# Performance work log

Hardware: AMD Instinct MI355X
Metric: run time of the kernel (lower is better)

Reference implementation:

```python
import jax, jax.numpy as jnp
import numpy as np

NUM_USERS = 50000
NUM_ITEMS = 100000
EMB_DIM = 64
N_LAYERS = 3
N_EDGES = 1200000
N_NODES = NUM_USERS + NUM_ITEMS


def setup_inputs() -> dict:
    key = jax.random.key(0)
    k1, k2, k3, k4, k5 = jax.random.split(key, 5)
    user_emb = jax.random.normal(k1, (NUM_USERS, EMB_DIM), dtype=jnp.float32)
    item_emb = jax.random.normal(k2, (NUM_ITEMS, EMB_DIM), dtype=jnp.float32)
    adj_rows = jax.random.randint(k3, (N_EDGES,), 0, N_NODES, dtype=jnp.int32)
    adj_cols = jax.random.randint(k4, (N_EDGES,), 0, N_NODES, dtype=jnp.int32)
    adj_vals = jax.random.uniform(k5, (N_EDGES,), dtype=jnp.float32)
    return {"user_emb": user_emb, "item_emb": item_emb,
            "adj_rows": adj_rows, "adj_cols": adj_cols, "adj_vals": adj_vals}


def reference(user_emb, item_emb, adj_rows, adj_cols, adj_vals):
    num_users = user_emb.shape[0]
    n_nodes = num_users + item_emb.shape[0]

    def spmm(x):
        # y[r] += v * x[c] for each nnz (r, c, v)  -- COO SpMM
        msgs = adj_vals[:, None] * x[adj_cols]          # [E, D]
        return jax.ops.segment_sum(msgs, adj_rows, num_segments=n_nodes)

    all_emb = jnp.concatenate([user_emb, item_emb], axis=0)  # [N, D]
    # fused multi-hop propagation: accumulate layer outputs instead of stacking
    acc = all_emb
    for _ in range(N_LAYERS):
        all_emb = spmm(all_emb)
        acc = acc + all_emb
    final_embs = acc / jnp.float32(N_LAYERS + 1)  # mean over (n_layers+1) hops
    users = final_embs[:num_users]
    items = final_embs[num_users:]
    return (users, items)
```

## Files before the change

kernel.cpp:

```cpp
#include <hip/hip_runtime.h>
#include <hip/hip_cooperative_groups.h>

namespace cg = cooperative_groups;

#define EMB 64
#define BKT_BITS 9
#define BKT_ROWS (1 << BKT_BITS)
#define BKT_CAP 4608
#define MAX_BKT 512
#define CO_EDGES 2048

typedef float f32x4 __attribute__((ext_vector_type(4)));
typedef int int4e __attribute__((ext_vector_type(4), aligned(8)));


__device__ __forceinline__ const float4* xrow(const float* xu,
                                              const float* xi,
                                              int nu, int col) {
    return (const float4*)((col < nu) ? (xu + (size_t)col * EMB)
                                      : (xi + (size_t)(col - nu) * EMB));
}

__device__ void coarse_body(const int* __restrict__ rows,
                            const int* __restrict__ cols,
                            const float* __restrict__ vals,
                            int* bcur, int2* __restrict__ es_raw,
                            int n_edges, int nbkt,
                            int* lcnt, int* lbase,
                            int cstart, int cstride) {
    int tid = threadIdx.x;
    int nchunk = (n_edges + CO_EDGES - 1) / CO_EDGES;
    for (int c = cstart; c < nchunk; c += cstride) {
        for (int i = tid; i < nbkt; i += 512) lcnt[i] = 0;
        __syncthreads();
        int e0 = c * CO_EDGES;
        int e1 = min(e0 + CO_EDGES, n_edges);
        for (int e = e0 + tid; e < e1; e += 512)
            atomicAdd(&lcnt[rows[e] >> BKT_BITS], 1);
        __syncthreads();
        for (int i = tid; i < nbkt; i += 512) {
            int cc = lcnt[i];
            lbase[i] = cc ? atomicAdd(&bcur[i], cc) : 0;
        }
        __syncthreads();
        for (int e = e0 + tid; e < e1; e += 512) {
            int r = rows[e];
            int b = r >> BKT_BITS;
            int p = atomicAdd(&lbase[b], 1);
            if (p < BKT_CAP)
                es_raw[(size_t)b * BKT_CAP + p] =
                    make_int2(cols[e] | ((r & (BKT_ROWS - 1)) << 18),
                              __float_as_int(vals[e]));
        }
        __syncthreads();
    }
}

__device__ void fine_body(const int* bcur,
                          const int2* __restrict__ es_raw,
                          int2* __restrict__ es,
                          int2* __restrict__ rbe, int n_nodes, int nbkt,
                          int* rcnt, int* rsc,
                          int bstart, int bstride) {
    int tid = threadIdx.x;
    for (int b = bstart; b < nbkt; b += bstride) {
        int cnt = min(bcur[b], BKT_CAP);
        int base = b * BKT_CAP;
        rcnt[tid] = 0;
        __syncthreads();
        for (int j = tid; j < cnt; j += BKT_ROWS)
            atomicAdd(&rcnt[es_raw[base + j].x >> 18], 1);
        __syncthreads();
        int v = rcnt[tid];
        rsc[tid] = v;
        __syncthreads();
        for (int d = 1; d < BKT_ROWS; d <<= 1) {
            int t = (tid >= d) ? rsc[tid - d] : 0;
            __syncthreads();
            rsc[tid] += t;
            __syncthreads();
        }
        int excl = rsc[tid] - v;
        rcnt[tid] = excl;
        int r = (b << BKT_BITS) + tid;
        if (r < n_nodes) rbe[r] = make_int2(base + excl, base + excl + v);
        __syncthreads();
        for (int j = tid; j < cnt; j += BKT_ROWS) {
            int2 e = es_raw[base + j];
            int p = atomicAdd(&rcnt[e.x >> 18], 1);
            es[base + p] = make_int2(e.x & 0x3FFFF, e.y);
        }
        __syncthreads();
    }
}

__device__ void spmm_body(const int2* __restrict__ rbe,
                          const int2* __restrict__ es,
                          const float* xu, const float* xi, int nu,
                          float4* y, const float4* y1, const float4* y2,
                          const float* __restrict__ x0u,
                          const float* __restrict__ x0i,
                          int n_nodes, int mode, int gid0, int gstride) {
    int lanes = n_nodes * 16;
    for (int gid = gid0; gid < lanes; gid += gstride) {
        int r = gid >> 4;
        int q = gid & 15;
        int2 be = rbe[r];
        int beg = be.x;
        int end = be.y;
        float4 a = make_float4(0.f, 0.f, 0.f, 0.f);
        int j = beg;
        for (; j + 4 <= end; j += 4) {
            int4e p01 = *(const int4e*)(es + j);
            int4e p23 = *(const int4e*)(es + j + 2);
            const float4* r0 = xrow(xu, xi, nu, p01.x);
            const float4* r1 = xrow(xu, xi, nu, p01.z);
            const float4* r2 = xrow(xu, xi, nu, p23.x);
            const float4* r3 = xrow(xu, xi, nu, p23.z);
            float4 x0 = r0[q];
            float4 x1 = r1[q];
            float4 x2 = r2[q];
            float4 x3 = r3[q];
            float v0 = __int_as_float(p01.y);
            float v1 = __int_as_float(p01.w);
            float v2 = __int_as_float(p23.y);
            float v3 = __int_as_float(p23.w);
            a.x += v0 * x0.x; a.y += v0 * x0.y; a.z += v0 * x0.z; a.w += v0 * x0.w;
            a.x += v1 * x1.x; a.y += v1 * x1.y; a.z += v1 * x1.z; a.w += v1 * x1.w;
            a.x += v2 * x2.x; a.y += v2 * x2.y; a.z += v2 * x2.z; a.w += v2 * x2.w;
            a.x += v3 * x3.x; a.y += v3 * x3.y; a.z += v3 * x3.z; a.w += v3 * x3.w;
        }
        if (j + 2 <= end) {
            int4e p01 = *(const int4e*)(es + j);
            const float4* r0 = xrow(xu, xi, nu, p01.x);
            const float4* r1 = xrow(xu, xi, nu, p01.z);
            float4 x0 = r0[q];
            float4 x1 = r1[q];
            float v0 = __int_as_float(p01.y);
            float v1 = __int_as_float(p01.w);
            a.x += v0 * x0.x; a.y += v0 * x0.y; a.z += v0 * x0.z; a.w += v0 * x0.w;
            a.x += v1 * x1.x; a.y += v1 * x1.y; a.z += v1 * x1.z; a.w += v1 * x1.w;
            j += 2;
        }
        if (j < end) {
            int2 e0 = es[j];
            float4 x0 = xrow(xu, xi, nu, e0.x)[q];
            float v0 = __int_as_float(e0.y);
            a.x += v0 * x0.x; a.y += v0 * x0.y; a.z += v0 * x0.z; a.w += v0 * x0.w;
        }
        size_t o = (size_t)r * (EMB / 4) + q;
        if (mode < 2) {
            y[o] = a;
        } else {
            const float4* b0 = (r < nu)
                ? ((const float4*)x0u + (size_t)r * (EMB / 4))
                : ((const float4*)x0i + (size_t)(r - nu) * (EMB / 4));
            float4 f0 = b0[q];
            float4 a1 = y1[o];
            float4 a2 = y2[o];
            float4 ac;
            ac.x = 0.25f * (f0.x + a1.x + a2.x + a.x);
            ac.y = 0.25f * (f0.y + a1.y + a2.y + a.y);
            ac.z = 0.25f * (f0.z + a1.z + a2.z + a.z);
            ac.w = 0.25f * (f0.w + a1.w + a2.w + a.w);
            __builtin_nontemporal_store(*(const f32x4*)&ac, (f32x4*)&y[o]);
        }
    }
}

__global__ __launch_bounds__(512) void mega(
        const int* __restrict__ rows, const int* __restrict__ cols,
        const float* __restrict__ vals,
        int* bcur, int2* __restrict__ es_raw, int2* __restrict__ es,
        int2* __restrict__ rbe,
        const float* __restrict__ ue, const float* __restrict__ ie,
        float* y2buf, float* out,
        int nu, int n_nodes, int n_edges, int nbkt) {
    cg::grid_group grid = cg::this_grid();
    __shared__ int lcnt[MAX_BKT];
    __shared__ int lbase[MAX_BKT];
    __shared__ int rcnt[BKT_ROWS];
    __shared__ int rsc[BKT_ROWS];
    int gid0 = blockIdx.x * blockDim.x + threadIdx.x;
    int gstride = gridDim.x * blockDim.x;

    coarse_body(rows, cols, vals, bcur, es_raw, n_edges, nbkt,
                lcnt, lbase, blockIdx.x, gridDim.x);
    grid.sync();

    fine_body(bcur, es_raw, es, rbe, n_nodes, nbkt, rcnt, rsc,
              blockIdx.x, gridDim.x);
    grid.sync();

    spmm_body(rbe, es, ue, ie, nu, (float4*)out,
              nullptr, nullptr, nullptr, nullptr, n_nodes, 0, gid0, gstride);
    grid.sync();

    spmm_body(rbe, es, out, out + (size_t)nu * EMB, nu, (float4*)y2buf,
              nullptr, nullptr, nullptr, nullptr, n_nodes, 1, gid0, gstride);
    grid.sync();

    spmm_body(rbe, es, y2buf, y2buf + (size_t)nu * EMB, nu, (float4*)out,
              (const float4*)out, (const float4*)y2buf, ue, ie,
              n_nodes, 2, gid0, gstride);
}


__global__ __launch_bounds__(512) void k_coarse(
        const int* __restrict__ rows, const int* __restrict__ cols,
        const float* __restrict__ vals, int* bcur, int2* __restrict__ es_raw,
        int n_edges, int nbkt) {
    __shared__ int lcnt[MAX_BKT];
    __shared__ int lbase[MAX_BKT];
    coarse_body(rows, cols, vals, bcur, es_raw, n_edges, nbkt,
                lcnt, lbase, blockIdx.x, gridDim.x);
}

__global__ __launch_bounds__(512) void k_fine(
        const int* bcur, const int2* __restrict__ es_raw,
        int2* __restrict__ es, int2* __restrict__ rbe,
        int n_nodes, int nbkt) {
    __shared__ int rcnt[BKT_ROWS];
    __shared__ int rsc[BKT_ROWS];
    fine_body(bcur, es_raw, es, rbe, n_nodes, nbkt, rcnt, rsc,
              blockIdx.x, gridDim.x);
}

__global__ __launch_bounds__(256) void k_spmm(
        const int2* __restrict__ rbe, const int2* __restrict__ es,
        const float* xu, const float* xi, int nu,
        float4* y, const float4* y1, const float4* y2,
        const float* __restrict__ x0u, const float* __restrict__ x0i,
        int n_nodes, int mode) {
    spmm_body(rbe, es, xu, xi, nu, y, y1, y2, x0u, x0i, n_nodes, mode,
              blockIdx.x * blockDim.x + threadIdx.x,
              gridDim.x * blockDim.x);
}

extern "C" void kernel_launch(void* const* d_in, const int* in_sizes, int n_in,
                              void* d_out, int out_size, void* d_ws, size_t ws_size,
                              hipStream_t stream) {
    const float* ue   = (const float*)d_in[0];
    const float* ie   = (const float*)d_in[1];
    const int*   rows = (const int*)d_in[2];
    const int*   cols = (const int*)d_in[3];
    const float* vals = (const float*)d_in[4];
    float* out = (float*)d_out;

    const int num_users = in_sizes[0] / EMB;
    const int num_items = in_sizes[1] / EMB;
    const int n_nodes   = num_users + num_items;
    const int n_edges   = in_sizes[2];
    const int nbkt      = (n_nodes + BKT_ROWS - 1) >> BKT_BITS;

    const size_t buf_elems = (size_t)n_nodes * EMB;
    float* y2buf  = (float*)d_ws;
    int2*  es     = (int2*)(y2buf + buf_elems);
    int2*  es_raw = es + (size_t)nbkt * BKT_CAP;
    int2*  rbe    = es_raw + (size_t)nbkt * BKT_CAP;
    int*   bcur   = (int*)(rbe + n_nodes);

    int occ = 0, cus = 0, dev = 0;
    hipGetDevice(&dev);
    hipOccupancyMaxActiveBlocksPerMultiprocessor(&occ, mega, 512, 0);
    hipDeviceGetAttribute(&cus, hipDeviceAttributeMultiprocessorCount, dev);
    if (cus < 1) cus = 256;
    if (occ > 4) occ = 4;

    hipMemsetAsync(bcur, 0, (size_t)nbkt * sizeof(int), stream);

    bool done = false;
    if (occ >= 3) {
        int grid_blocks = occ * cus;
        int nu = num_users, nn = n_nodes, ne = n_edges, nb = nbkt;
        void* args[] = { (void*)&rows, (void*)&cols, (void*)&vals,
                         (void*)&bcur, (void*)&es_raw, (void*)&es,
                         (void*)&rbe, (void*)&ue, (void*)&ie,
                         (void*)&y2buf, (void*)&out,
                         (void*)&nu, (void*)&nn, (void*)&ne, (void*)&nb };
        hipError_t err = hipLaunchCooperativeKernel(
            mega, dim3(grid_blocks), dim3(512), args, 0, stream);
        done = (err == hipSuccess);
        if (!done) (void)hipGetLastError();
    }

    if (!done) {
        int nchunk = (n_edges + CO_EDGES - 1) / CO_EDGES;
        k_coarse<<<nchunk, 512, 0, stream>>>(rows, cols, vals, bcur, es_raw,
                                             n_edges, nbkt);
        k_fine<<<nbkt, 512, 0, stream>>>(bcur, es_raw, es, rbe,
                                         n_nodes, nbkt);
        int blocks = (n_nodes * 16 + 255) / 256;
        k_spmm<<<blocks, 256, 0, stream>>>(
            rbe, es, ue, ie, num_users, (float4*)out,
            nullptr, nullptr, nullptr, nullptr, n_nodes, 0);
        k_spmm<<<blocks, 256, 0, stream>>>(
            rbe, es, (const float*)out,
            (const float*)out + (size_t)num_users * EMB, num_users,
            (float4*)y2buf, nullptr, nullptr, nullptr, nullptr, n_nodes, 1);
        k_spmm<<<blocks, 256, 0, stream>>>(
            rbe, es, y2buf, y2buf + (size_t)num_users * EMB, num_users,
            (float4*)out, (const float4*)out, (const float4*)y2buf,
            ue, ie, n_nodes, 2);
    }
}
```

Measured before the change: 284.8 us.

## Store gathered embeddings and intermediate layers in fp16 to halve gather traffic

The input embeddings are converted to fp16 in the first phase, and the intermediate layer outputs are kept in fp16. Each SpMM gathers 8 bytes per lane instead of 16 and accumulates in fp32. This targets the memory bandwidth spent on random row gathers. In exchange it adds a conversion pass and loses precision, which may exceed the tolerance. The final output is still written in fp32.

```diff
diff --git a/kernel.cpp b/kernel.cpp
--- a/kernel.cpp
+++ b/kernel.cpp
@@ -1,4 +1,5 @@
 #include <hip/hip_runtime.h>
+#include <hip/hip_fp16.h>
 #include <hip/hip_cooperative_groups.h>
 
 namespace cg = cooperative_groups;
@@ -12,13 +13,20 @@
 
 typedef float f32x4 __attribute__((ext_vector_type(4)));
 typedef int int4e __attribute__((ext_vector_type(4), aligned(8)));
-
-
-__device__ __forceinline__ const float4* xrow(const float* xu,
-                                              const float* xi,
-                                              int nu, int col) {
-    return (const float4*)((col < nu) ? (xu + (size_t)col * EMB)
-                                      : (xi + (size_t)(col - nu) * EMB));
+typedef unsigned short ushort_t;
+
+
+__device__ void convert_body(const float4* __restrict__ ue4,
+                             const float4* __restrict__ ie4,
+                             int nu16, uint2* __restrict__ xh2,
+                             int lanes, int gid0, int gstride) {
+    for (int o = gid0; o < lanes; o += gstride) {
+        float4 v = (o < nu16) ? ue4[o] : ie4[o - nu16];
+        __half2 lo = __floats2half2_rn(v.x, v.y);
+        __half2 hi = __floats2half2_rn(v.z, v.w);
+        xh2[o] = make_uint2(__builtin_bit_cast(unsigned, lo),
+                            __builtin_bit_cast(unsigned, hi));
+    }
 }
 
 __device__ void coarse_body(const int* __restrict__ rows,
@@ -94,76 +102,80 @@
     }
 }
 
+__device__ __forceinline__ void fmad_h(float4& a, float v, uint2 g) {
+    __half2 h0 = __builtin_bit_cast(__half2, g.x);
+    __half2 h1 = __builtin_bit_cast(__half2, g.y);
+    float2 f0 = __half22float2(h0);
+    float2 f1 = __half22float2(h1);
+    a.x += v * f0.x; a.y += v * f0.y; a.z += v * f1.x; a.w += v * f1.y;
+}
+
 __device__ void spmm_body(const int2* __restrict__ rbe,
                           const int2* __restrict__ es,
-                          const float* xu, const float* xi, int nu,
-                          float4* y, const float4* y1, const float4* y2,
+                          const ushort_t* __restrict__ xh,
+                          ushort_t* __restrict__ yh,
+                          const ushort_t* __restrict__ y1h,
+                          const ushort_t* __restrict__ y2h,
                           const float* __restrict__ x0u,
-                          const float* __restrict__ x0i,
+                          const float* __restrict__ x0i, int nu,
+                          float4* __restrict__ out,
                           int n_nodes, int mode, int gid0, int gstride) {
     int lanes = n_nodes * 16;
     for (int gid = gid0; gid < lanes; gid += gstride) {
         int r = gid >> 4;
         int q = gid & 15;
         int2 be = rbe[r];
-        int beg = be.x;
+        int j = be.x;
         int end = be.y;
         float4 a = make_float4(0.f, 0.f, 0.f, 0.f);
-        int j = beg;
         for (; j + 4 <= end; j += 4) {
             int4e p01 = *(const int4e*)(es + j);
             int4e p23 = *(const int4e*)(es + j + 2);
-            const float4* r0 = xrow(xu, xi, nu, p01.x);
-            const float4* r1 = xrow(xu, xi, nu, p01.z);
-            const float4* r2 = xrow(xu, xi, nu, p23.x);
-            const float4* r3 = xrow(xu, xi, nu, p23.z);
-            float4 x0 = r0[q];
-            float4 x1 = r1[q];
-            float4 x2 = r2[q];
-            float4 x3 = r3[q];
-            float v0 = __int_as_float(p01.y);
-            float v1 = __int_as_float(p01.w);
-            float v2 = __int_as_float(p23.y);
-            float v3 = __int_as_float(p23.w);
-            a.x += v0 * x0.x; a.y += v0 * x0.y; a.z += v0 * x0.z; a.w += v0 * x0.w;
-            a.x += v1 * x1.x; a.y += v1 * x1.y; a.z += v1 * x1.z; a.w += v1 * x1.w;
-            a.x += v2 * x2.x; a.y += v2 * x2.y; a.z += v2 * x2.z; a.w += v2 * x2.w;
-            a.x += v3 * x3.x; a.y += v3 * x3.y; a.z += v3 * x3.z; a.w += v3 * x3.w;
+            uint2 g0 = *((const uint2*)(xh + (size_t)p01.x * EMB) + q);
+            uint2 g1 = *((const uint2*)(xh + (size_t)p01.z * EMB) + q);
+            uint2 g2 = *((const uint2*)(xh + (size_t)p23.x * EMB) + q);
+            uint2 g3 = *((const uint2*)(xh + (size_t)p23.z * EMB) + q);
+            fmad_h(a, __int_as_float(p01.y), g0);
+            fmad_h(a, __int_as_float(p01.w), g1);
+            fmad_h(a, __int_as_float(p23.y), g2);
+            fmad_h(a, __int_as_float(p23.w), g3);
         }
         if (j + 2 <= end) {
             int4e p01 = *(const int4e*)(es + j);
-            const float4* r0 = xrow(xu, xi, nu, p01.x);
-            const float4* r1 = xrow(xu, xi, nu, p01.z);
-            float4 x0 = r0[q];
-            float4 x1 = r1[q];
-            float v0 = __int_as_float(p01.y);
-            float v1 = __int_as_float(p01.w);
-            a.x += v0 * x0.x; a.y += v0 * x0.y; a.z += v0 * x0.z; a.w += v0 * x0.w;
-            a.x += v1 * x1.x; a.y += v1 * x1.y; a.z += v1 * x1.z; a.w += v1 * x1.w;
+            uint2 g0 = *((const uint2*)(xh + (size_t)p01.x * EMB) + q);
+            uint2 g1 = *((const uint2*)(xh + (size_t)p01.z * EMB) + q);
+            fmad_h(a, __int_as_float(p01.y), g0);
+            fmad_h(a, __int_as_float(p01.w), g1);
             j += 2;
         }
         if (j < end) {
             int2 e0 = es[j];
-            float4 x0 = xrow(xu, xi, nu, e0.x)[q];
-            float v0 = __int_as_float(e0.y);
-            a.x += v0 * x0.x; a.y += v0 * x0.y; a.z += v0 * x0.z; a.w += v0 * x0.w;
-        }
-        size_t o = (size_t)r * (EMB / 4) + q;
+            uint2 g0 = *((const uint2*)(xh + (size_t)e0.x * EMB) + q);
+            fmad_h(a, __int_as_float(e0.y), g0);
+        }
+        size_t o = (size_t)r * 16 + q;
         if (mode < 2) {
-            y[o] = a;
+            __half2 lo = __floats2half2_rn(a.x, a.y);
+            __half2 hi = __floats2half2_rn(a.z, a.w);
+            ((uint2*)yh)[o] = make_uint2(__builtin_bit_cast(unsigned, lo),
+                                         __builtin_bit_cast(unsigned, hi));
         } else {
+            uint2 u1 = ((const uint2*)y1h)[o];
+            uint2 u2 = ((const uint2*)y2h)[o];
+            float2 c1l = __half22float2(__builtin_bit_cast(__half2, u1.x));
+            float2 c1h = __half22float2(__builtin_bit_cast(__half2, u1.y));
+            float2 c2l = __half22float2(__builtin_bit_cast(__half2, u2.x));
+            float2 c2h = __half22float2(__builtin_bit_cast(__half2, u2.y));
             const float4* b0 = (r < nu)
-                ? ((const float4*)x0u + (size_t)r * (EMB / 4))
-                : ((const float4*)x0i + (size_t)(r - nu) * (EMB / 4));
+                ? ((const float4*)x0u + (size_t)r * 16)
+                : ((const float4*)x0i + (size_t)(r - nu) * 16);
             float4 f0 = b0[q];
-            float4 a1 = y1[o];
-            float4 a2 = y2[o];
-            float4 ac;
-            ac.x = 0.25f * (f0.x + a1.x + a2.x + a.x);
-            ac.y = 0.25f * (f0.y + a1.y + a2.y + a.y);
-            ac.z = 0.25f * (f0.z + a1.z + a2.z + a.z);
-            ac.w = 0.25f * (f0.w + a1.w + a2.w + a.w);
-            __builtin_nontemporal_store(*(const f32x4*)&ac, (f32x4*)&y[o]);
+            f32x4 ac;
+            ac.x = 0.25f * (f0.x + c1l.x + c2l.x + a.x);
+            ac.y = 0.25f * (f0.y + c1l.y + c2l.y + a.y);
+            ac.z = 0.25f * (f0.z + c1h.x + c2h.x + a.z);
+            ac.w = 0.25f * (f0.w + c1h.y + c2h.y + a.w);
+            __builtin_nontemporal_store(ac, (f32x4*)&out[o]);
         }
     }
 }
@@ -174,7 +186,7 @@
         int* bcur, int2* __restrict__ es_raw, int2* __restrict__ es,
         int2* __restrict__ rbe,
         const float* __restrict__ ue, const float* __restrict__ ie,
-        float* y2buf, float* out,
+        ushort_t* xh, ushort_t* y1h, ushort_t* y2h, float* out,
         int nu, int n_nodes, int n_edges, int nbkt) {
     cg::grid_group grid = cg::this_grid();
     __shared__ int lcnt[MAX_BKT];
@@ -184,6 +196,8 @@
     int gid0 = blockIdx.x * blockDim.x + threadIdx.x;
     int gstride = gridDim.x * blockDim.x;
 
+    convert_body((const float4*)ue, (const float4*)ie, nu * 16,
+                 (uint2*)xh, n_nodes * 16, gid0, gstride);
     coarse_body(rows, cols, vals, bcur, es_raw, n_edges, nbkt,
                 lcnt, lbase, blockIdx.x, gridDim.x);
     grid.sync();
@@ -192,26 +206,30 @@
               blockIdx.x, gridDim.x);
     grid.sync();
 
-    spmm_body(rbe, es, ue, ie, nu, (float4*)out,
-              nullptr, nullptr, nullptr, nullptr, n_nodes, 0, gid0, gstride);
+    spmm_body(rbe, es, xh, y1h, nullptr, nullptr, nullptr, nullptr, nu,
+              nullptr, n_nodes, 0, gid0, gstride);
     grid.sync();
 
-    spmm_body(rbe, es, out, out + (size_t)nu * EMB, nu, (float4*)y2buf,
-              nullptr, nullptr, nullptr, nullptr, n_nodes, 1, gid0, gstride);
+    spmm_body(rbe, es, y1h, y2h, nullptr, nullptr, nullptr, nullptr, nu,
+              nullptr, n_nodes, 1, gid0, gstride);
     grid.sync();
 
-    spmm_body(rbe, es, y2buf, y2buf + (size_t)nu * EMB, nu, (float4*)out,
-              (const float4*)out, (const float4*)y2buf, ue, ie,
-              n_nodes, 2, gid0, gstride);
+    spmm_body(rbe, es, y2h, nullptr, y1h, y2h, ue, ie, nu,
+              (float4*)out, n_nodes, 2, gid0, gstride);
 }
 
 
 __global__ __launch_bounds__(512) void k_coarse(
         const int* __restrict__ rows, const int* __restrict__ cols,
         const float* __restrict__ vals, int* bcur, int2* __restrict__ es_raw,
-        int n_edges, int nbkt) {
+        const float* __restrict__ ue, const float* __restrict__ ie,
+        ushort_t* xh, int nu, int n_nodes, int n_edges, int nbkt) {
     __shared__ int lcnt[MAX_BKT];
     __shared__ int lbase[MAX_BKT];
+    int gid0 = blockIdx.x * blockDim.x + threadIdx.x;
+    int gstride = gridDim.x * blockDim.x;
+    convert_body((const float4*)ue, (const float4*)ie, nu * 16,
+                 (uint2*)xh, n_nodes * 16, gid0, gstride);
     coarse_body(rows, cols, vals, bcur, es_raw, n_edges, nbkt,
                 lcnt, lbase, blockIdx.x, gridDim.x);
 }
@@ -228,11 +246,11 @@
 
 __global__ __launch_bounds__(256) void k_spmm(
         const int2* __restrict__ rbe, const int2* __restrict__ es,
-        const float* xu, const float* xi, int nu,
-        float4* y, const float4* y1, const float4* y2,
-        const float* __restrict__ x0u, const float* __restrict__ x0i,
-        int n_nodes, int mode) {
-    spmm_body(rbe, es, xu, xi, nu, y, y1, y2, x0u, x0i, n_nodes, mode,
+        const ushort_t* xh, ushort_t* yh,
+        const ushort_t* y1h, const ushort_t* y2h,
+        const float* x0u, const float* x0i, int nu,
+        float4* out, int n_nodes, int mode) {
+    spmm_body(rbe, es, xh, yh, y1h, y2h, x0u, x0i, nu, out, n_nodes, mode,
               blockIdx.x * blockDim.x + threadIdx.x,
               gridDim.x * blockDim.x);
 }
@@ -254,8 +272,10 @@
     const int nbkt      = (n_nodes + BKT_ROWS - 1) >> BKT_BITS;
 
     const size_t buf_elems = (size_t)n_nodes * EMB;
-    float* y2buf  = (float*)d_ws;
-    int2*  es     = (int2*)(y2buf + buf_elems);
+    ushort_t* xh  = (ushort_t*)d_ws;
+    ushort_t* y1h = xh + buf_elems;
+    ushort_t* y2h = y1h + buf_elems;
+    int2*  es     = (int2*)(y2h + buf_elems);
     int2*  es_raw = es + (size_t)nbkt * BKT_CAP;
     int2*  rbe    = es_raw + (size_t)nbkt * BKT_CAP;
     int*   bcur   = (int*)(rbe + n_nodes);
@@ -276,7 +296,7 @@
         void* args[] = { (void*)&rows, (void*)&cols, (void*)&vals,
                          (void*)&bcur, (void*)&es_raw, (void*)&es,
                          (void*)&rbe, (void*)&ue, (void*)&ie,
-                         (void*)&y2buf, (void*)&out,
+                         (void*)&xh, (void*)&y1h, (void*)&y2h, (void*)&out,
                          (void*)&nu, (void*)&nn, (void*)&ne, (void*)&nb };
         hipError_t err = hipLaunchCooperativeKernel(
             mega, dim3(grid_blocks), dim3(512), args, 0, stream);
@@ -287,20 +307,19 @@
     if (!done) {
         int nchunk = (n_edges + CO_EDGES - 1) / CO_EDGES;
         k_coarse<<<nchunk, 512, 0, stream>>>(rows, cols, vals, bcur, es_raw,
-                                             n_edges, nbkt);
+                                             ue, ie, xh, num_users,
+                                             n_nodes, n_edges, nbkt);
         k_fine<<<nbkt, 512, 0, stream>>>(bcur, es_raw, es, rbe,
                                          n_nodes, nbkt);
         int blocks = (n_nodes * 16 + 255) / 256;
         k_spmm<<<blocks, 256, 0, stream>>>(
-            rbe, es, ue, ie, num_users, (float4*)out,
-            nullptr, nullptr, nullptr, nullptr, n_nodes, 0);
+            rbe, es, xh, y1h, nullptr, nullptr, nullptr, nullptr,
+            num_users, nullptr, n_nodes, 0);
         k_spmm<<<blocks, 256, 0, stream>>>(
-            rbe, es, (const float*)out,
-            (const float*)out + (size_t)num_users * EMB, num_users,
-            (float4*)y2buf, nullptr, nullptr, nullptr, nullptr, n_nodes, 1);
+            rbe, es, y1h, y2h, nullptr, nullptr, nullptr, nullptr,
+            num_users, nullptr, n_nodes, 1);
         k_spmm<<<blocks, 256, 0, stream>>>(
-            rbe, es, y2buf, y2buf + (size_t)num_users * EMB, num_users,
-            (float4*)out, (const float4*)out, (const float4*)y2buf,
-            ue, ie, n_nodes, 2);
-    }
-}
+            rbe, es, y2h, nullptr, y1h, y2h, ue, ie,
+            num_users, (float4*)out, n_nodes, 2);
+    }
+}
```

Measured after the change: 240.0 us. 15.7% less time.
